# Kernel optimization log

Measured on AMD Instinct MI355X. Metric: run time of the kernel, lower is better.

The kernel has to match this reference:

```python
import jax, jax.numpy as jnp
import numpy as np

B, C, N, S = 4, 64, 16384, 16
DIM_OUT = 64
SCALE = DIM_OUT ** (-0.5)


def setup_inputs() -> dict:
    key = jax.random.key(0)
    ks = jax.random.split(key, 8)
    return {
        "xyz": jax.random.normal(ks[0], (B, 3, N), dtype=jnp.float32),
        "neighbor_xyz": jax.random.normal(ks[1], (B, 3, N, S), dtype=jnp.float32),
        "points": jax.random.normal(ks[2], (B, C, N), dtype=jnp.float32),
        "neighbor_points": jax.random.normal(ks[3], (B, C, N, S), dtype=jnp.float32),
        "Wk": jax.random.normal(ks[4], (C, C), dtype=jnp.float32) * 0.05,
        "Wv": jax.random.normal(ks[5], (DIM_OUT, C + 3), dtype=jnp.float32) * 0.05,
        "Wp": jax.random.normal(ks[6], (C, 4), dtype=jnp.float32) * 0.05,
        "bp": jax.random.normal(ks[7], (C,), dtype=jnp.float32) * 0.05,
    }


def reference(xyz, neighbor_xyz, points, neighbor_points, Wk, Wv, Wp, bp):
    # relative position of each neighbor: [B,3,N,S]
    tmp = xyz[:, :, :, None] - neighbor_xyz
    xyz_norm = jnp.sqrt(jnp.sum(tmp * tmp, axis=1, keepdims=True))  # [B,1,N,S]
    pos = jnp.concatenate([tmp, xyz_norm], axis=1)  # [B,4,N,S]

    # 1x1 convs == per-point channel matmuls
    pos_enc = jnp.einsum('oc,bcns->bons', Wp, pos) + bp[None, :, None, None]
    k = jnp.einsum('oc,bcns->bons', Wk, neighbor_points + pos_enc)  # [B,C,N,S]
    v_in = jnp.concatenate([neighbor_points, tmp], axis=1)  # [B,C+3,N,S]
    v = jnp.einsum('oc,bcns->bons', Wv, v_in)  # [B,dim_out,N,S]

    q = points * SCALE  # [B,C,N]
    attn = jax.nn.softmax(jnp.einsum('bcn,bcns->bns', q, k), axis=-1)  # [B,N,S]
    out = jnp.einsum('bns,bcns->bcn', attn, v)  # [B,dim_out,N]
    return out
```

## Files before the change

### kernel.cpp

```cpp
#include <hip/hip_runtime.h>
#include <math.h>

constexpr int Nn = 16384;
constexpr int ST = 68;
constexpr size_t NS = (size_t)Nn * 16;

template <int CTRL>
__device__ __forceinline__ float dpp_f(float x) {
    return __int_as_float(
        __builtin_amdgcn_update_dpp(0, __float_as_int(x), CTRL, 0xF, 0xF, false));
}
__device__ __forceinline__ float rsum16(float v) {
    v += dpp_f<0x128>(v); v += dpp_f<0x124>(v);
    v += dpp_f<0x122>(v); v += dpp_f<0x121>(v);
    return v;
}
__device__ __forceinline__ float rmax16(float v) {
    v = fmaxf(v, dpp_f<0x128>(v)); v = fmaxf(v, dpp_f<0x124>(v));
    v = fmaxf(v, dpp_f<0x122>(v)); v = fmaxf(v, dpp_f<0x121>(v));
    return v;
}

__global__ __launch_bounds__(256, 4) void qkpp_kernel(
    const float* __restrict__ points, const float* __restrict__ Wk,
    const float* __restrict__ Wp, float* __restrict__ ws)
{
    const int tid = threadIdx.x;
    const int lane = tid & 63;
    const int q = lane >> 4;
    const int pt = blockIdx.x * 64 + (tid >> 6) * 16 + (lane & 15);
    const int b = pt >> 14;
    const int n = pt & (Nn - 1);

    float qk[16];
#pragma unroll
    for (int k = 0; k < 16; ++k) qk[k] = 0.f;

    const float* prow = points + (size_t)b * 64 * Nn + n;
    const float* wkq = Wk + 16 * q;
#pragma unroll 4
    for (int c = 0; c < 64; ++c) {
        const float qv = prow[(size_t)c * Nn];
        const float4 w0 = *(const float4*)(wkq + c * 64 + 0);
        const float4 w1 = *(const float4*)(wkq + c * 64 + 4);
        const float4 w2 = *(const float4*)(wkq + c * 64 + 8);
        const float4 w3 = *(const float4*)(wkq + c * 64 + 12);
        qk[0]  = fmaf(qv, w0.x, qk[0]);  qk[1]  = fmaf(qv, w0.y, qk[1]);
        qk[2]  = fmaf(qv, w0.z, qk[2]);  qk[3]  = fmaf(qv, w0.w, qk[3]);
        qk[4]  = fmaf(qv, w1.x, qk[4]);  qk[5]  = fmaf(qv, w1.y, qk[5]);
        qk[6]  = fmaf(qv, w1.z, qk[6]);  qk[7]  = fmaf(qv, w1.w, qk[7]);
        qk[8]  = fmaf(qv, w2.x, qk[8]);  qk[9]  = fmaf(qv, w2.y, qk[9]);
        qk[10] = fmaf(qv, w2.z, qk[10]); qk[11] = fmaf(qv, w2.w, qk[11]);
        qk[12] = fmaf(qv, w3.x, qk[12]); qk[13] = fmaf(qv, w3.y, qk[13]);
        qk[14] = fmaf(qv, w3.z, qk[14]); qk[15] = fmaf(qv, w3.w, qk[15]);
    }
#pragma unroll
    for (int k = 0; k < 16; ++k) qk[k] *= 0.125f;

    float p0 = 0.f, p1 = 0.f, p2 = 0.f, p3 = 0.f;
#pragma unroll
    for (int k = 0; k < 16; ++k) {
        const float4 wp4 = *(const float4*)(Wp + (16 * q + k) * 4);
        p0 = fmaf(qk[k], wp4.x, p0);
        p1 = fmaf(qk[k], wp4.y, p1);
        p2 = fmaf(qk[k], wp4.z, p2);
        p3 = fmaf(qk[k], wp4.w, p3);
    }
    p0 += __shfl_xor(p0, 16); p0 += __shfl_xor(p0, 32);
    p1 += __shfl_xor(p1, 16); p1 += __shfl_xor(p1, 32);
    p2 += __shfl_xor(p2, 16); p2 += __shfl_xor(p2, 32);
    p3 += __shfl_xor(p3, 16); p3 += __shfl_xor(p3, 32);

    float* orow = ws + (size_t)pt * ST + 16 * q;
    ((float4*)orow)[0] = make_float4(qk[0],  qk[1],  qk[2],  qk[3]);
    ((float4*)orow)[1] = make_float4(qk[4],  qk[5],  qk[6],  qk[7]);
    ((float4*)orow)[2] = make_float4(qk[8],  qk[9],  qk[10], qk[11]);
    ((float4*)orow)[3] = make_float4(qk[12], qk[13], qk[14], qk[15]);
    if (q == 0)
        *(float4*)(ws + (size_t)pt * ST + 64) = make_float4(p0, p1, p2, p3);
}

__global__ __launch_bounds__(256, 4) void attn_out_kernel(
    const float* __restrict__ xyz, const float* __restrict__ nxyz,
    const float* __restrict__ npts, const float* __restrict__ Wv,
    const float* __restrict__ ws, float* __restrict__ out)
{
    __shared__ float wvT[67 * 68];

    const int tid = threadIdx.x;
    for (int idx = tid; idx < 64 * 67; idx += 256) {
        const int o = idx / 67, c = idx - o * 67;
        wvT[c * 68 + o] = Wv[idx];
    }
    __syncthreads();

    const int lane = tid & 63;
    const int s = lane & 15;
    const int nn = lane >> 4;
    const int gpt = blockIdx.x * 16 + (tid >> 6) * 4;
    const int b = gpt >> 14;
    const int ng = gpt & (Nn - 1);
    const int pt = gpt + nn;

    const float* npb = npts + (size_t)(b * 64) * NS + (size_t)ng * 16 + lane;

    float npv[64];
#pragma unroll
    for (int c = 0; c < 64; ++c) npv[c] = npb[(size_t)c * NS];

    const float nx0 = nxyz[((size_t)(b * 3 + 0) * Nn + ng) * 16 + lane];
    const float nx1 = nxyz[((size_t)(b * 3 + 1) * Nn + ng) * 16 + lane];
    const float nx2 = nxyz[((size_t)(b * 3 + 2) * Nn + ng) * 16 + lane];
    const float x0 = xyz[(size_t)(b * 3 + 0) * Nn + ng + nn];
    const float x1 = xyz[(size_t)(b * 3 + 1) * Nn + ng + nn];
    const float x2 = xyz[(size_t)(b * 3 + 2) * Nn + ng + nn];
    const float d0 = x0 - nx0, d1 = x1 - nx1, d2 = x2 - nx2;
    const float dn = sqrtf(d0 * d0 + d1 * d1 + d2 * d2);

    const float* qrow = ws + (size_t)pt * ST;

    float l0 = 0.f, l1 = 0.f, l2 = 0.f, l3 = 0.f;
#pragma unroll
    for (int jc = 0; jc < 16; ++jc) {
        const float4 qq = *(const float4*)(qrow + 4 * jc);
        l0 = fmaf(qq.x, npv[4 * jc + 0], l0);
        l1 = fmaf(qq.y, npv[4 * jc + 1], l1);
        l2 = fmaf(qq.z, npv[4 * jc + 2], l2);
        l3 = fmaf(qq.w, npv[4 * jc + 3], l3);
    }
    const float4 ppv = *(const float4*)(qrow + 64);
    float logit = (l0 + l1) + (l2 + l3);
    logit += ppv.x * d0 + ppv.y * d1 + ppv.z * d2 + ppv.w * dn;

    const float mx = rmax16(logit);
    const float e = __expf(logit - mx);
    const float se = rsum16(e);
    const float attn = e / se;

    float a0 = 0.f, a1 = 0.f, a2 = 0.f, a3 = 0.f;
#pragma unroll
    for (int c = 0; c < 64; ++c) {
        const float r = rsum16(attn * npv[c]);
        const float4 wq = *(const float4*)&wvT[c * 68 + 4 * s];
        a0 = fmaf(r, wq.x, a0);
        a1 = fmaf(r, wq.y, a1);
        a2 = fmaf(r, wq.z, a2);
        a3 = fmaf(r, wq.w, a3);
    }
    {
        const float t0 = rsum16(attn * d0);
        const float t1 = rsum16(attn * d1);
        const float t2 = rsum16(attn * d2);
        const float4 wA = *(const float4*)&wvT[64 * 68 + 4 * s];
        const float4 wB = *(const float4*)&wvT[65 * 68 + 4 * s];
        const float4 wC = *(const float4*)&wvT[66 * 68 + 4 * s];
        a0 = fmaf(t0, wA.x, a0); a1 = fmaf(t0, wA.y, a1);
        a2 = fmaf(t0, wA.z, a2); a3 = fmaf(t0, wA.w, a3);
        a0 = fmaf(t1, wB.x, a0); a1 = fmaf(t1, wB.y, a1);
        a2 = fmaf(t1, wB.z, a2); a3 = fmaf(t1, wB.w, a3);
        a0 = fmaf(t2, wC.x, a0); a1 = fmaf(t2, wC.y, a1);
        a2 = fmaf(t2, wC.z, a2); a3 = fmaf(t2, wC.w, a3);
    }

    float* ob = out + ((size_t)(b * 64 + 4 * s) * Nn) + ng + nn;
    ob[0]          = a0;
    ob[(size_t)Nn]     = a1;
    ob[(size_t)Nn * 2] = a2;
    ob[(size_t)Nn * 3] = a3;
}

extern "C" void kernel_launch(void* const* d_in, const int* in_sizes, int n_in,
                              void* d_out, int out_size, void* d_ws, size_t ws_size,
                              hipStream_t stream) {
    const float* xyz    = (const float*)d_in[0];
    const float* nxyz   = (const float*)d_in[1];
    const float* points = (const float*)d_in[2];
    const float* npts   = (const float*)d_in[3];
    const float* Wk     = (const float*)d_in[4];
    const float* Wv     = (const float*)d_in[5];
    const float* Wp     = (const float*)d_in[6];
    float* out = (float*)d_out;
    float* ws = (float*)d_ws;

    hipLaunchKernelGGL(qkpp_kernel,     dim3(1024), dim3(256), 0, stream,
                       points, Wk, Wp, ws);
    hipLaunchKernelGGL(attn_out_kernel, dim3(4096), dim3(256), 0, stream,
                       xyz, nxyz, npts, Wv, ws, out);
}
```

Baseline: 118.1 us.

## Stage neighbor features into LDS via direct global-to-LDS loads, pack Wv as bf16

The attention kernel now copies each block's 64x256 neighbor-feature tile straight into shared memory with global_load_lds instead of holding 64 registers per thread. The block's q/pos rows are also staged in LDS. Wv is packed as bf16 pairs in LDS to halve LDS traffic for weight reads, at the cost of lower-precision weights. The launch bound drops to 2 blocks per CU because LDS use grows to about 73KB per block, which may reduce latency hiding.

```diff
diff --git a/kernel.cpp b/kernel.cpp
--- a/kernel.cpp
+++ b/kernel.cpp
@@ -2,7 +2,6 @@
 #include <math.h>
 
 constexpr int Nn = 16384;
-constexpr int ST = 68;
 constexpr size_t NS = (size_t)Nn * 16;
 
 template <int CTRL>
@@ -20,6 +19,12 @@
     v = fmaxf(v, dpp_f<0x122>(v)); v = fmaxf(v, dpp_f<0x121>(v));
     return v;
 }
+
+__device__ __forceinline__ unsigned bf16_rne(unsigned u) {
+    return (u + 0x7FFFu + ((u >> 16) & 1u)) >> 16;
+}
+__device__ __forceinline__ float blo(unsigned u) { return __uint_as_float(u << 16); }
+__device__ __forceinline__ float bhi(unsigned u) { return __uint_as_float(u & 0xFFFF0000u); }
 
 __global__ __launch_bounds__(256, 4) void qkpp_kernel(
     const float* __restrict__ points, const float* __restrict__ Wk,
@@ -71,102 +76,113 @@
     p2 += __shfl_xor(p2, 16); p2 += __shfl_xor(p2, 32);
     p3 += __shfl_xor(p3, 16); p3 += __shfl_xor(p3, 32);
 
-    float* orow = ws + (size_t)pt * ST + 16 * q;
+    float* orow = ws + (size_t)pt * 68 + 16 * q;
     ((float4*)orow)[0] = make_float4(qk[0],  qk[1],  qk[2],  qk[3]);
     ((float4*)orow)[1] = make_float4(qk[4],  qk[5],  qk[6],  qk[7]);
     ((float4*)orow)[2] = make_float4(qk[8],  qk[9],  qk[10], qk[11]);
     ((float4*)orow)[3] = make_float4(qk[12], qk[13], qk[14], qk[15]);
     if (q == 0)
-        *(float4*)(ws + (size_t)pt * ST + 64) = make_float4(p0, p1, p2, p3);
-}
-
-__global__ __launch_bounds__(256, 4) void attn_out_kernel(
+        *(float4*)(ws + (size_t)pt * 68 + 64) = make_float4(p0, p1, p2, p3);
+}
+
+__global__ __launch_bounds__(256, 2) void attn_stream_kernel(
     const float* __restrict__ xyz, const float* __restrict__ nxyz,
     const float* __restrict__ npts, const float* __restrict__ Wv,
     const float* __restrict__ ws, float* __restrict__ out)
 {
-    __shared__ float wvT[67 * 68];
-
-    const int tid = threadIdx.x;
-    for (int idx = tid; idx < 64 * 67; idx += 256) {
-        const int o = idx / 67, c = idx - o * 67;
-        wvT[c * 68 + o] = Wv[idx];
-    }
-    __syncthreads();
-
-    const int lane = tid & 63;
-    const int s = lane & 15;
-    const int nn = lane >> 4;
-    const int gpt = blockIdx.x * 16 + (tid >> 6) * 4;
+    __shared__ float np_lds[64 * 256];
+    __shared__ __align__(16) float qk_lds[16 * 68];
+    __shared__ __align__(16) unsigned wvP[34 * 68];
+
+    const int t = threadIdx.x;
+    const int w = t >> 6;
+    const int l = t & 63;
+    const int s = t & 15;
+    const int p = t >> 4;
+    const int gpt = blockIdx.x * 16;
     const int b = gpt >> 14;
-    const int ng = gpt & (Nn - 1);
-    const int pt = gpt + nn;
-
-    const float* npb = npts + (size_t)(b * 64) * NS + (size_t)ng * 16 + lane;
-
-    float npv[64];
-#pragma unroll
-    for (int c = 0; c < 64; ++c) npv[c] = npb[(size_t)c * NS];
-
-    const float nx0 = nxyz[((size_t)(b * 3 + 0) * Nn + ng) * 16 + lane];
-    const float nx1 = nxyz[((size_t)(b * 3 + 1) * Nn + ng) * 16 + lane];
-    const float nx2 = nxyz[((size_t)(b * 3 + 2) * Nn + ng) * 16 + lane];
-    const float x0 = xyz[(size_t)(b * 3 + 0) * Nn + ng + nn];
-    const float x1 = xyz[(size_t)(b * 3 + 1) * Nn + ng + nn];
-    const float x2 = xyz[(size_t)(b * 3 + 2) * Nn + ng + nn];
+    const int n0 = gpt & (Nn - 1);
+
+    {
+        const float* src0 = npts + (size_t)(b * 64 + 16 * w) * NS + (size_t)n0 * 16 + 4 * l;
+        float* dst0 = np_lds + (16 * w) * 256;
+#pragma unroll
+        for (int k = 0; k < 16; ++k) {
+            __builtin_amdgcn_global_load_lds(src0 + (size_t)k * NS, dst0 + k * 256, 16, 0, 0);
+        }
+    }
+
+    for (int i = t; i < 16 * 68; i += 256)
+        qk_lds[i] = ws[(size_t)gpt * 68 + i];
+
+    for (int i = t; i < 64 * 34; i += 256) {
+        const int o = i / 34, cp = i - o * 34;
+        const int c0 = 2 * cp;
+        const unsigned ulo = __float_as_uint(Wv[o * 67 + c0]);
+        const unsigned uhi = (c0 + 1 < 67) ? __float_as_uint(Wv[o * 67 + c0 + 1]) : 0u;
+        wvP[cp * 68 + o] = bf16_rne(ulo) | (bf16_rne(uhi) << 16);
+    }
+
+    const float nx0 = nxyz[((size_t)(b * 3 + 0) * Nn + n0) * 16 + t];
+    const float nx1 = nxyz[((size_t)(b * 3 + 1) * Nn + n0) * 16 + t];
+    const float nx2 = nxyz[((size_t)(b * 3 + 2) * Nn + n0) * 16 + t];
+    const float x0 = xyz[(size_t)(b * 3 + 0) * Nn + n0 + p];
+    const float x1 = xyz[(size_t)(b * 3 + 1) * Nn + n0 + p];
+    const float x2 = xyz[(size_t)(b * 3 + 2) * Nn + n0 + p];
     const float d0 = x0 - nx0, d1 = x1 - nx1, d2 = x2 - nx2;
     const float dn = sqrtf(d0 * d0 + d1 * d1 + d2 * d2);
 
-    const float* qrow = ws + (size_t)pt * ST;
-
+    __syncthreads();
+
+    const float* qrow = qk_lds + p * 68;
     float l0 = 0.f, l1 = 0.f, l2 = 0.f, l3 = 0.f;
 #pragma unroll
-    for (int jc = 0; jc < 16; ++jc) {
-        const float4 qq = *(const float4*)(qrow + 4 * jc);
-        l0 = fmaf(qq.x, npv[4 * jc + 0], l0);
-        l1 = fmaf(qq.y, npv[4 * jc + 1], l1);
-        l2 = fmaf(qq.z, npv[4 * jc + 2], l2);
-        l3 = fmaf(qq.w, npv[4 * jc + 3], l3);
-    }
-    const float4 ppv = *(const float4*)(qrow + 64);
+    for (int c4 = 0; c4 < 16; ++c4) {
+        const float4 qq = ((const float4*)qrow)[c4];
+        l0 = fmaf(qq.x, np_lds[(4 * c4 + 0) * 256 + t], l0);
+        l1 = fmaf(qq.y, np_lds[(4 * c4 + 1) * 256 + t], l1);
+        l2 = fmaf(qq.z, np_lds[(4 * c4 + 2) * 256 + t], l2);
+        l3 = fmaf(qq.w, np_lds[(4 * c4 + 3) * 256 + t], l3);
+    }
+    const float4 pp = ((const float4*)qrow)[16];
     float logit = (l0 + l1) + (l2 + l3);
-    logit += ppv.x * d0 + ppv.y * d1 + ppv.z * d2 + ppv.w * dn;
+    logit += pp.x * d0 + pp.y * d1 + pp.z * d2 + pp.w * dn;
 
     const float mx = rmax16(logit);
     const float e = __expf(logit - mx);
     const float se = rsum16(e);
     const float attn = e / se;
 
-    float a0 = 0.f, a1 = 0.f, a2 = 0.f, a3 = 0.f;
-#pragma unroll
-    for (int c = 0; c < 64; ++c) {
-        const float r = rsum16(attn * npv[c]);
-        const float4 wq = *(const float4*)&wvT[c * 68 + 4 * s];
-        a0 = fmaf(r, wq.x, a0);
-        a1 = fmaf(r, wq.y, a1);
-        a2 = fmaf(r, wq.z, a2);
-        a3 = fmaf(r, wq.w, a3);
+    float4 oa = make_float4(0.f, 0.f, 0.f, 0.f);
+#pragma unroll
+    for (int cp = 0; cp < 32; ++cp) {
+        const float n0v = np_lds[(2 * cp + 0) * 256 + t];
+        const float n1v = np_lds[(2 * cp + 1) * 256 + t];
+        const float r0 = rsum16(attn * n0v);
+        const float r1 = rsum16(attn * n1v);
+        const uint4 wq = *(const uint4*)&wvP[cp * 68 + 4 * s];
+        oa.x = fmaf(r0, blo(wq.x), oa.x); oa.x = fmaf(r1, bhi(wq.x), oa.x);
+        oa.y = fmaf(r0, blo(wq.y), oa.y); oa.y = fmaf(r1, bhi(wq.y), oa.y);
+        oa.z = fmaf(r0, blo(wq.z), oa.z); oa.z = fmaf(r1, bhi(wq.z), oa.z);
+        oa.w = fmaf(r0, blo(wq.w), oa.w); oa.w = fmaf(r1, bhi(wq.w), oa.w);
     }
     {
         const float t0 = rsum16(attn * d0);
         const float t1 = rsum16(attn * d1);
         const float t2 = rsum16(attn * d2);
-        const float4 wA = *(const float4*)&wvT[64 * 68 + 4 * s];
-        const float4 wB = *(const float4*)&wvT[65 * 68 + 4 * s];
-        const float4 wC = *(const float4*)&wvT[66 * 68 + 4 * s];
-        a0 = fmaf(t0, wA.x, a0); a1 = fmaf(t0, wA.y, a1);
-        a2 = fmaf(t0, wA.z, a2); a3 = fmaf(t0, wA.w, a3);
-        a0 = fmaf(t1, wB.x, a0); a1 = fmaf(t1, wB.y, a1);
-        a2 = fmaf(t1, wB.z, a2); a3 = fmaf(t1, wB.w, a3);
-        a0 = fmaf(t2, wC.x, a0); a1 = fmaf(t2, wC.y, a1);
-        a2 = fmaf(t2, wC.z, a2); a3 = fmaf(t2, wC.w, a3);
-    }
-
-    float* ob = out + ((size_t)(b * 64 + 4 * s) * Nn) + ng + nn;
-    ob[0]          = a0;
-    ob[(size_t)Nn]     = a1;
-    ob[(size_t)Nn * 2] = a2;
-    ob[(size_t)Nn * 3] = a3;
+        const uint4 wqa = *(const uint4*)&wvP[32 * 68 + 4 * s];
+        const uint4 wqb = *(const uint4*)&wvP[33 * 68 + 4 * s];
+        oa.x += t0 * blo(wqa.x) + t1 * bhi(wqa.x) + t2 * blo(wqb.x);
+        oa.y += t0 * blo(wqa.y) + t1 * bhi(wqa.y) + t2 * blo(wqb.y);
+        oa.z += t0 * blo(wqa.z) + t1 * bhi(wqa.z) + t2 * blo(wqb.z);
+        oa.w += t0 * blo(wqa.w) + t1 * bhi(wqa.w) + t2 * blo(wqb.w);
+    }
+
+    float* ob = out + ((size_t)(b * 64 + 4 * s)) * Nn + n0 + p;
+    ob[0]              = oa.x;
+    ob[(size_t)Nn]     = oa.y;
+    ob[(size_t)Nn * 2] = oa.z;
+    ob[(size_t)Nn * 3] = oa.w;
 }
 
 extern "C" void kernel_launch(void* const* d_in, const int* in_sizes, int n_in,
@@ -182,8 +198,8 @@
     float* out = (float*)d_out;
     float* ws = (float*)d_ws;
 
-    hipLaunchKernelGGL(qkpp_kernel,     dim3(1024), dim3(256), 0, stream,
+    hipLaunchKernelGGL(qkpp_kernel,        dim3(1024), dim3(256), 0, stream,
                        points, Wk, Wp, ws);
-    hipLaunchKernelGGL(attn_out_kernel, dim3(4096), dim3(256), 0, stream,
+    hipLaunchKernelGGL(attn_stream_kernel, dim3(4096), dim3(256), 0, stream,
                        xyz, nxyz, npts, Wv, ws, out);
 }
```

Result: slower. 150.7 us (+27.5%).
